# Performance work log

Hardware: AMD Instinct MI355X
Metric: run time of the kernel (lower is better)

## Reference

```python
import jax, jax.numpy as jnp
import numpy as np

B, S, D, H = 2, 2048, 512, 8
DK = D // H  # 64


def setup_inputs() -> dict:
    key = jax.random.key(0)
    ks = jax.random.split(key, 16)
    def t(k):
        return jax.random.normal(k, (B, S, D), dtype=jnp.float32)
    inp = {
        'query_real': t(ks[0]), 'key_real': t(ks[1]), 'value_real': t(ks[2]),
        'query_phase': t(ks[3]), 'key_phase': t(ks[4]), 'value_phase': t(ks[5]),
        'mask': jax.random.randint(ks[6], (B, 1, S), 0, 2, dtype=jnp.int32),
    }
    # Four distinct linear layers (clones deepcopies); real and phase paths share them.
    for i, nm in enumerate(['q', 'k', 'v', 'o']):
        inp['W' + nm] = jax.random.normal(ks[7 + 2 * i], (D, D), dtype=jnp.float32) * 0.02
        inp['b' + nm] = jax.random.normal(ks[8 + 2 * i], (D,), dtype=jnp.float32) * 0.02
    return inp


def _lin(x, W, b):
    # nn.Linear: x @ W.T + b
    return jnp.einsum('bsd,ed->bse', x, W) + b


def _heads(x):
    # [B,S,D] -> [B,H,S,DK]
    return jnp.swapaxes(x.reshape(B, S, H, DK), 1, 2)


def reference(query_real, key_real, value_real, query_phase, key_phase, value_phase,
              mask, Wq, bq, Wk, bk, Wv, bv, Wo, bo):
    qr = _heads(_lin(query_real, Wq, bq)); qp = _heads(_lin(query_phase, Wq, bq))
    kr = _heads(_lin(key_real, Wk, bk));   kp = _heads(_lin(key_phase, Wk, bk))
    vr = _heads(_lin(value_real, Wv, bv)); vp = _heads(_lin(value_phase, Wv, bv))

    # complex QK^T: 4 matmuls -> real/imag parts, magnitude score
    sr = jnp.einsum('bhqd,bhkd->bhqk', qr, kr) - jnp.einsum('bhqd,bhkd->bhqk', qp, kp)
    sp = jnp.einsum('bhqd,bhkd->bhqk', qr, kp) + jnp.einsum('bhqd,bhkd->bhqk', qp, kr)
    scores = jnp.sqrt(sr * sr + sp * sp) / jnp.sqrt(jnp.float32(DK))
    # mask [B,1,S] -> unsqueeze head dim -> [B,1,1,S]
    scores = jnp.where(mask[:, None] == 0, jnp.float32(-1e9), scores)
    p = jax.nn.softmax(scores, axis=-1)

    xr = jnp.einsum('bhqk,bhkd->bhqd', p, vr)
    xp = jnp.einsum('bhqk,bhkd->bhqd', p, vp)
    xr = jnp.swapaxes(xr, 1, 2).reshape(B, S, D)
    xp = jnp.swapaxes(xp, 1, 2).reshape(B, S, D)
    return _lin(xr, Wo, bo), _lin(xp, Wo, bo)
```

## Files before the change

### kernel.cpp

```cpp
#include <hip/hip_runtime.h>

typedef __bf16 bf16;
typedef __bf16 bf16x8 __attribute__((ext_vector_type(8)));
typedef float  f32x4  __attribute__((ext_vector_type(4)));

static constexpr int CB = 2;
static constexpr int CS = 2048;
static constexpr int CD = 512;
static constexpr int CH = 8;
static constexpr int CDK = 64;
static constexpr int NROWS = CB * CH * CS;
static constexpr size_t NT = (size_t)CB * CS * CD;
static constexpr size_t WN = (size_t)CD * CD;

__device__ __forceinline__ f32x4 mfma16(bf16x8 a, bf16x8 b, f32x4 c) {
    return __builtin_amdgcn_mfma_f32_16x16x32_bf16(a, b, c, 0, 0, 0);
}

__device__ __forceinline__ bf16x8 cvt8(const float* __restrict__ p) {
    float4 x0 = *reinterpret_cast<const float4*>(p);
    float4 x1 = *reinterpret_cast<const float4*>(p + 4);
    bf16x8 r;
    r[0] = (bf16)x0.x; r[1] = (bf16)x0.y; r[2] = (bf16)x0.z; r[3] = (bf16)x0.w;
    r[4] = (bf16)x1.x; r[5] = (bf16)x1.y; r[6] = (bf16)x1.z; r[7] = (bf16)x1.w;
    return r;
}

__device__ __forceinline__ void gload16(const void* g, void* l) {
    __builtin_amdgcn_global_load_lds(
        (const __attribute__((address_space(1))) void*)g,
        (__attribute__((address_space(3))) void*)l, 16, 0, 0);
}

struct CvtP {
    const float* src[10];
    bf16* dst[10];
    int n8[10];
};
__global__ __launch_bounds__(256) void cvt_kernel(CvtP C) {
    const int t = blockIdx.y;
    const int i = blockIdx.x * 256 + threadIdx.x;
    if (i < C.n8[t])
        *reinterpret_cast<bf16x8*>(C.dst[t] + (size_t)i * 8) =
            cvt8(C.src[t] + (size_t)i * 8);
}

struct PB {
    const bf16* A[6];
    const bf16* W[6];
    const float* bias[6];
    bf16* dst[6];
    int mode[6];
};
__global__ __launch_bounds__(256) void projb_kernel(PB P) {
    __shared__ uint4 tile[2][2][512];

    const int z = blockIdx.z;
    const bf16* __restrict__ A = P.A[z];
    const bf16* __restrict__ W = P.W[z];
    const float* __restrict__ bias = P.bias[z];
    bf16* __restrict__ dst = P.dst[z];
    const int mode = P.mode[z];

    const int m0 = blockIdx.x * 64, n0 = blockIdx.y * 64;
    const int tid = threadIdx.x;
    const int lane = tid & 63, w = tid >> 6;
    const int wm = w >> 1, wn = w & 1;
    const int l16 = lane & 15, lhi = lane >> 4;

    const int tensor = w >> 1, half = w & 1;
    const int rlo = lane >> 3, slotL = lane & 7;
    const bf16* gbase = tensor ? W : A;
    const int t0 = tensor ? n0 : m0;
    const char* gp = (const char*)gbase
                   + (size_t)(t0 + half*32 + rlo) * (CD * 2)
                   + (size_t)((slotL ^ rlo) * 16);

    auto stage = [&](int buf, int kk) {
        const char* p = gp + (size_t)kk * 128;
        uint4* ld = &tile[buf][tensor][half * 256];
        #pragma unroll
        for (int i = 0; i < 4; ++i)
            gload16(p + (size_t)i * 8 * (CD * 2), ld + i * 64);
    };

    f32x4 acc[2][2] = {};

    stage(0, 0);
    asm volatile("s_waitcnt vmcnt(0)" ::: "memory");
    __syncthreads();

    for (int kk = 0; kk < 8; ++kk) {
        if (kk + 1 < 8) stage((kk + 1) & 1, kk + 1);

        const uint4* aT = &tile[kk & 1][0][0];
        const uint4* bT = &tile[kk & 1][1][0];
        #pragma unroll
        for (int ks = 0; ks < 2; ++ks) {
            const int c = ks*4 + lhi;
            const int ra0 = wm*32 + l16, ra1 = ra0 + 16;
            const int rb0 = wn*32 + l16, rb1 = rb0 + 16;
            bf16x8 af0 = __builtin_bit_cast(bf16x8, aT[ra0*8 + (c ^ (ra0 & 7))]);
            bf16x8 af1 = __builtin_bit_cast(bf16x8, aT[ra1*8 + (c ^ (ra1 & 7))]);
            bf16x8 bg0 = __builtin_bit_cast(bf16x8, bT[rb0*8 + (c ^ (rb0 & 7))]);
            bf16x8 bg1 = __builtin_bit_cast(bf16x8, bT[rb1*8 + (c ^ (rb1 & 7))]);
            acc[0][0] = mfma16(af0, bg0, acc[0][0]);
            acc[0][1] = mfma16(af0, bg1, acc[0][1]);
            acc[1][0] = mfma16(af1, bg0, acc[1][0]);
            acc[1][1] = mfma16(af1, bg1, acc[1][1]);
        }
        if (kk + 1 < 8) __syncthreads();
    }

    #pragma unroll
    for (int ms = 0; ms < 2; ++ms)
    #pragma unroll
    for (int ns = 0; ns < 2; ++ns) {
        const int col = n0 + wn*32 + ns*16 + l16;
        const float bv = bias[col];
        const int hh = col >> 6, dk = col & 63;
        #pragma unroll
        for (int i = 0; i < 4; ++i) {
            const int m = m0 + wm*32 + ms*16 + lhi*4 + i;
            const float v = acc[ms][ns][i] + bv;
            const int b = m >> 11, s = m & 2047;
            if (mode == 0)
                dst[(((size_t)(b*CH + hh)) * CS + s) * CDK + dk] = (bf16)v;
            else
                dst[(((size_t)(b*CH + hh)) * CDK + dk) * CS + s] = (bf16)v;
        }
    }
}

__global__ __launch_bounds__(256) void oprojb_kernel(
    const bf16* __restrict__ Xr, const bf16* __restrict__ Xp,
    const bf16* __restrict__ Wo, const float* __restrict__ bo,
    float* __restrict__ out)
{
    __shared__ uint4 tile[2][2][512];

    const bf16* __restrict__ A = blockIdx.z ? Xp : Xr;
    float* __restrict__ dst = out + (size_t)blockIdx.z * NT;

    const int m0 = blockIdx.x * 64, n0 = blockIdx.y * 64;
    const int tid = threadIdx.x;
    const int lane = tid & 63, w = tid >> 6;
    const int wm = w >> 1, wn = w & 1;
    const int l16 = lane & 15, lhi = lane >> 4;

    const int tensor = w >> 1, half = w & 1;
    const int rlo = lane >> 3, slotL = lane & 7;
    const bf16* gbase = tensor ? Wo : A;
    const int t0 = tensor ? n0 : m0;
    const char* gp = (const char*)gbase
                   + (size_t)(t0 + half*32 + rlo) * (CD * 2)
                   + (size_t)((slotL ^ rlo) * 16);

    auto stage = [&](int buf, int kk) {
        const char* p = gp + (size_t)kk * 128;
        uint4* ld = &tile[buf][tensor][half * 256];
        #pragma unroll
        for (int i = 0; i < 4; ++i)
            gload16(p + (size_t)i * 8 * (CD * 2), ld + i * 64);
    };

    f32x4 acc[2][2] = {};

    stage(0, 0);
    asm volatile("s_waitcnt vmcnt(0)" ::: "memory");
    __syncthreads();

    for (int kk = 0; kk < 8; ++kk) {
        if (kk + 1 < 8) stage((kk + 1) & 1, kk + 1);

        const uint4* aT = &tile[kk & 1][0][0];
        const uint4* bT = &tile[kk & 1][1][0];
        #pragma unroll
        for (int ks = 0; ks < 2; ++ks) {
            const int c = ks*4 + lhi;
            const int ra0 = wm*32 + l16, ra1 = ra0 + 16;
            const int rb0 = wn*32 + l16, rb1 = rb0 + 16;
            bf16x8 af0 = __builtin_bit_cast(bf16x8, aT[ra0*8 + (c ^ (ra0 & 7))]);
            bf16x8 af1 = __builtin_bit_cast(bf16x8, aT[ra1*8 + (c ^ (ra1 & 7))]);
            bf16x8 bg0 = __builtin_bit_cast(bf16x8, bT[rb0*8 + (c ^ (rb0 & 7))]);
            bf16x8 bg1 = __builtin_bit_cast(bf16x8, bT[rb1*8 + (c ^ (rb1 & 7))]);
            acc[0][0] = mfma16(af0, bg0, acc[0][0]);
            acc[0][1] = mfma16(af0, bg1, acc[0][1]);
            acc[1][0] = mfma16(af1, bg0, acc[1][0]);
            acc[1][1] = mfma16(af1, bg1, acc[1][1]);
        }
        if (kk + 1 < 8) __syncthreads();
    }

    #pragma unroll
    for (int ms = 0; ms < 2; ++ms)
    #pragma unroll
    for (int ns = 0; ns < 2; ++ns) {
        const int col = n0 + wn*32 + ns*16 + l16;
        const float bv = bo[col];
        #pragma unroll
        for (int i = 0; i < 4; ++i) {
            const int m = m0 + wm*32 + ms*16 + lhi*4 + i;
            dst[(size_t)m * 512 + col] = acc[ms][ns][i] + bv;
        }
    }
}

__global__ __launch_bounds__(256) void attn_kernel(
    const bf16* __restrict__ Qr, const bf16* __restrict__ Qp,
    const bf16* __restrict__ Kr, const bf16* __restrict__ Kp,
    const bf16* __restrict__ Vtr, const bf16* __restrict__ Vtp,
    const int* __restrict__ mask, int lognsp,
    float* __restrict__ POR, float* __restrict__ POP, float* __restrict__ PLs)
{
    __shared__ uint4 stg[2][4][512];

    const int F = blockIdx.x;
    const int qt = (F >> 3) & 15;
    const int g  = (F & 7) | ((F >> 7) << 3);
    const int bh = g >> lognsp, z = g & ((1 << lognsp) - 1);
    const int Lkv = CS >> lognsp, kvbase = z * Lkv;
    const int nt = Lkv >> 6;
    const int b = bh >> 3;
    const size_t base = (size_t)bh * CS * CDK;

    const int tid = threadIdx.x, lane = tid & 63, w = tid >> 6;
    const int l16 = lane & 15, lhi = lane >> 4;
    const int q0 = qt * 128 + w * 32;

    const int srowL = lane >> 3, slotL = lane & 7;
    const int chunkL = slotL ^ srowL;
    const char* gsrc;
    size_t laneoff, iStride, tStride;
    if (w == 0)      gsrc = (const char*)Kr;
    else if (w == 1) gsrc = (const char*)Kp;
    else if (w == 2) gsrc = (const char*)Vtr;
    else             gsrc = (const char*)Vtp;
    if (w < 2) {
        laneoff = base*2 + (size_t)(kvbase + srowL) * 128 + chunkL*16;
        iStride = 1024;  tStride = 8192;
    } else {
        laneoff = base*2 + (size_t)srowL * (CS*2) + (size_t)kvbase*2 + chunkL*16;
        iStride = 8 * CS * 2;  tStride = 128;
    }
    const char* gp = gsrc + laneoff;

    auto stage = [&](int bi, int t) {
        const char* p = gp + (size_t)t * tStride;
        uint4* ldst = &stg[bi][w][0];
        #pragma unroll
        for (int i = 0; i < 8; ++i)
            gload16(p + i*iStride, ldst + i*64);
    };

    stage(0, 0);

    bf16x8 qrf[2][2], qpf[2][2], qnf[2][2];
    #pragma unroll
    for (int ms = 0; ms < 2; ++ms)
        #pragma unroll
        for (int ks = 0; ks < 2; ++ks) {
            const size_t qoff = base + (size_t)(q0 + ms*16 + l16) * CDK + ks*32 + lhi*8;
            qrf[ms][ks] = *reinterpret_cast<const bf16x8*>(&Qr[qoff]);
            qpf[ms][ks] = *reinterpret_cast<const bf16x8*>(&Qp[qoff]);
            uint4 t = __builtin_bit_cast(uint4, qpf[ms][ks]);
            t.x ^= 0x80008000u; t.y ^= 0x80008000u; t.z ^= 0x80008000u; t.w ^= 0x80008000u;
            qnf[ms][ks] = __builtin_bit_cast(bf16x8, t);
        }

    unsigned long long keepA[8] = {};
    for (int t = 0; t < nt; ++t) {
        const unsigned long long m64 =
            __ballot(mask[b*CS + kvbase + t*64 + lane] != 0);
        const unsigned long long s = m64 >> (lhi * 4);
        const unsigned int k16 = (unsigned int)(s & 0xFull)
                               | ((unsigned int)((s >> 16) & 0xFull) << 4)
                               | ((unsigned int)((s >> 32) & 0xFull) << 8)
                               | ((unsigned int)((s >> 48) & 0xFull) << 12);
        keepA[t >> 2] |= (unsigned long long)k16 << ((t & 3) * 16);
    }

    f32x4 oR[2][4] = {}, oP[2][4] = {};
    float lpart[2] = {0.f, 0.f};

    asm volatile("s_waitcnt vmcnt(0)" ::: "memory");
    __syncthreads();

    for (int t = 0; t < nt; ++t) {
        if (t + 1 < nt) stage((t + 1) & 1, t + 1);

        const int bi = t & 1;
        const unsigned int k16 = (unsigned int)(keepA[t >> 2] >> ((t & 3) * 16)) & 0xFFFFu;
        const uint4* kTr = &stg[bi][0][0];
        const uint4* kTp = &stg[bi][1][0];
        const uint4* vTr = &stg[bi][2][0];
        const uint4* vTp = &stg[bi][3][0];

        #pragma unroll
        for (int ms = 0; ms < 2; ++ms) {
            float pp[4][4];
            #pragma unroll
            for (int kb = 0; kb < 4; ++kb) {
                const int krow = kb*16 + l16;
                f32x4 aR = {}, aP = {};
                __builtin_amdgcn_s_setprio(1);
                #pragma unroll
                for (int ks = 0; ks < 2; ++ks) {
                    const int ci = krow*8 + ((ks*4 + lhi) ^ (krow & 7));
                    const bf16x8 kr8 = __builtin_bit_cast(bf16x8, kTr[ci]);
                    const bf16x8 kp8 = __builtin_bit_cast(bf16x8, kTp[ci]);
                    aR = mfma16(kr8, qrf[ms][ks], aR);
                    aR = mfma16(kp8, qnf[ms][ks], aR);
                    aP = mfma16(kr8, qpf[ms][ks], aP);
                    aP = mfma16(kp8, qrf[ms][ks], aP);
                }
                __builtin_amdgcn_s_setprio(0);
                #pragma unroll
                for (int i = 0; i < 4; ++i) {
                    const float sr = aR[i], sp = aP[i];
                    const float mag = __builtin_amdgcn_sqrtf(fmaf(sr, sr, sp*sp));
                    float p = __builtin_amdgcn_exp2f(fmaf(mag, 0.18033688f, -5.77078016f));
                    p = ((k16 >> (kb*4 + i)) & 1u) ? p : 0.0f;
                    pp[kb][i] = p;
                    lpart[ms] += p;
                }
            }
            #pragma unroll
            for (int c = 0; c < 2; ++c) {
                unsigned int r0, r1, r2, r3;
                asm("v_cvt_pk_bf16_f32 %0, %1, %2" : "=v"(r0) : "v"(pp[2*c][0]),   "v"(pp[2*c][1]));
                asm("v_cvt_pk_bf16_f32 %0, %1, %2" : "=v"(r1) : "v"(pp[2*c][2]),   "v"(pp[2*c][3]));
                asm("v_cvt_pk_bf16_f32 %0, %1, %2" : "=v"(r2) : "v"(pp[2*c+1][0]), "v"(pp[2*c+1][1]));
                asm("v_cvt_pk_bf16_f32 %0, %1, %2" : "=v"(r3) : "v"(pp[2*c+1][2]), "v"(pp[2*c+1][3]));
                asm volatile("v_permlane32_swap_b32 %0, %1" : "+v"(r0), "+v"(r2));
                asm volatile("v_permlane32_swap_b32 %0, %1" : "+v"(r1), "+v"(r3));
                asm volatile("v_permlane16_swap_b32 %0, %1" : "+v"(r0), "+v"(r2));
                asm volatile("v_permlane16_swap_b32 %0, %1" : "+v"(r1), "+v"(r3));
                uint4 fw; fw.x = r0; fw.y = r1; fw.z = r2; fw.w = r3;
                const bf16x8 pa = __builtin_bit_cast(bf16x8, fw);
                __builtin_amdgcn_s_setprio(1);
                #pragma unroll
                for (int dt = 0; dt < 4; ++dt) {
                    const int vrow = dt*16 + l16;
                    const int ci = vrow*8 + ((c*4 + lhi) ^ (vrow & 7));
                    oR[ms][dt] = mfma16(__builtin_bit_cast(bf16x8, vTr[ci]), pa, oR[ms][dt]);
                    oP[ms][dt] = mfma16(__builtin_bit_cast(bf16x8, vTp[ci]), pa, oP[ms][dt]);
                }
                __builtin_amdgcn_s_setprio(0);
            }
        }

        if (t + 1 < nt) __syncthreads();
    }

    #pragma unroll
    for (int ms = 0; ms < 2; ++ms) {
        float v = lpart[ms];
        v += __shfl_xor(v, 16);
        v += __shfl_xor(v, 32);
        lpart[ms] = v;
    }
    const int r0q = bh * CS + q0;
    if (lane < 16) {
        PLs[(size_t)z * NROWS + r0q + lane]      = lpart[0];
        PLs[(size_t)z * NROWS + r0q + 16 + lane] = lpart[1];
    }
    const size_t zo = (size_t)z * NROWS * 64;
    #pragma unroll
    for (int ms = 0; ms < 2; ++ms)
        #pragma unroll
        for (int dt = 0; dt < 4; ++dt) {
            const size_t off = zo + (size_t)(r0q + ms*16 + l16) * 64 + dt*16 + lhi*4;
            *reinterpret_cast<f32x4*>(&POR[off]) = oR[ms][dt];
            *reinterpret_cast<f32x4*>(&POP[off]) = oP[ms][dt];
        }
}

__global__ __launch_bounds__(256) void merge_kernel(
    const float* __restrict__ POR, const float* __restrict__ POP,
    const float* __restrict__ PLs, int nsp,
    bf16* __restrict__ Xr, bf16* __restrict__ Xp)
{
    const int idx = blockIdx.x * 256 + threadIdx.x;
    const int r = idx >> 4, c0 = (idx & 15) * 4;
    float l = 0.f;
    f32x4 orv = {}, opv = {};
    for (int zz = 0; zz < nsp; ++zz) {
        l += PLs[(size_t)zz * NROWS + r];
        const size_t o = (size_t)zz * NROWS * 64 + (size_t)r * 64 + c0;
        orv += *reinterpret_cast<const f32x4*>(&POR[o]);
        opv += *reinterpret_cast<const f32x4*>(&POP[o]);
    }
    const float inv = 1.f / l;
    const int bh = r >> 11, q = r & 2047;
    const int b = bh >> 3, h = bh & 7;
    const size_t off = ((size_t)(b*CS + q)) * CD + h*CDK + c0;
    bf16 vr[4], vp[4];
    #pragma unroll
    for (int j = 0; j < 4; ++j) { vr[j] = (bf16)(orv[j]*inv); vp[j] = (bf16)(opv[j]*inv); }
    *reinterpret_cast<uint2*>(&Xr[off]) = *reinterpret_cast<const uint2*>(vr);
    *reinterpret_cast<uint2*>(&Xp[off]) = *reinterpret_cast<const uint2*>(vp);
}

extern "C" void kernel_launch(void* const* d_in, const int* in_sizes, int n_in,
                              void* d_out, int out_size, void* d_ws, size_t ws_size,
                              hipStream_t stream) {
    const float* q_r = (const float*)d_in[0];
    const float* k_r = (const float*)d_in[1];
    const float* v_r = (const float*)d_in[2];
    const float* q_p = (const float*)d_in[3];
    const float* k_p = (const float*)d_in[4];
    const float* v_p = (const float*)d_in[5];
    const int*  mask = (const int*)d_in[6];
    const float* Wq = (const float*)d_in[7];  const float* bq = (const float*)d_in[8];
    const float* Wk = (const float*)d_in[9];  const float* bk = (const float*)d_in[10];
    const float* Wv = (const float*)d_in[11]; const float* bv = (const float*)d_in[12];
    const float* Wo = (const float*)d_in[13]; const float* bo = (const float*)d_in[14];
    float* out = (float*)d_out;

    bf16* ws = (bf16*)d_ws;
    bf16* Abf = ws;
    bf16* Wbf = ws + 6 * NT;
    bf16* Qr  = Wbf + 4 * WN;
    bf16 *Qp = Qr + NT, *Kr = Qp + NT, *Kp = Kr + NT;
    bf16 *Vtr = Kp + NT, *Vtp = Vtr + NT;
    bf16 *Xr = Vtp + NT, *Xp = Xr + NT;
    float* POR = (float*)(Xp + NT);

    const size_t fixedB = (14 * NT + 4 * WN) * sizeof(bf16);
    const size_t per_split = (size_t)NROWS * 64 * 4 * 2 + (size_t)NROWS * 4;
    int nsp, lognsp;
    if (ws_size >= fixedB + 2 * per_split) { nsp = 2; lognsp = 1; }
    else                                   { nsp = 1; lognsp = 0; }
    float* POP = POR + (size_t)nsp * NROWS * 64;
    float* PLs = POP + (size_t)nsp * NROWS * 64;

    dim3 blk(256);

    CvtP C;
    C.src[0]=q_r; C.src[1]=q_p; C.src[2]=k_r; C.src[3]=k_p; C.src[4]=v_r; C.src[5]=v_p;
    C.src[6]=Wq;  C.src[7]=Wk;  C.src[8]=Wv;  C.src[9]=Wo;
    for (int i = 0; i < 6; ++i) { C.dst[i] = Abf + (size_t)i * NT; C.n8[i] = (int)(NT / 8); }
    for (int i = 0; i < 4; ++i) { C.dst[6+i] = Wbf + (size_t)i * WN; C.n8[6+i] = (int)(WN / 8); }
    cvt_kernel<<<dim3((unsigned)(NT / 8 / 256), 10), blk, 0, stream>>>(C);

    PB P;
    for (int i = 0; i < 6; ++i) P.A[i] = Abf + (size_t)i * NT;
    P.W[0]=Wbf;      P.W[1]=Wbf;      P.W[2]=Wbf+WN;   P.W[3]=Wbf+WN;
    P.W[4]=Wbf+2*WN; P.W[5]=Wbf+2*WN;
    P.bias[0]=bq; P.bias[1]=bq; P.bias[2]=bk; P.bias[3]=bk; P.bias[4]=bv; P.bias[5]=bv;
    P.dst[0]=Qr; P.dst[1]=Qp; P.dst[2]=Kr; P.dst[3]=Kp; P.dst[4]=Vtr; P.dst[5]=Vtp;
    P.mode[0]=0; P.mode[1]=0; P.mode[2]=0; P.mode[3]=0; P.mode[4]=1; P.mode[5]=1;
    projb_kernel<<<dim3(64, 8, 6), blk, 0, stream>>>(P);

    attn_kernel<<<dim3(256 * nsp), blk, 0, stream>>>(Qr, Qp, Kr, Kp, Vtr, Vtp,
                                                     mask, lognsp, POR, POP, PLs);

    merge_kernel<<<dim3(NROWS * 16 / 256), blk, 0, stream>>>(POR, POP, PLs, nsp, Xr, Xp);

    oprojb_kernel<<<dim3(64, 8, 2), blk, 0, stream>>>(Xr, Xp, Wbf + 3 * WN, bo, out);
}
```

Before: 128.6 us.

## Split attention block into 8 waves of 16 query rows each

The attention kernel now runs 512 threads (8 waves) per block instead of 256, and each wave handles 16 query rows rather than 32. K/V tile staging is split so two waves load each tensor half. The aim is more waves in flight to hide the latency of the exp/sqrt and LDS reads, and fewer registers per wave. In exchange, each K/V fragment read from LDS is reused across fewer query rows, so LDS read traffic per MFMA doubles.

```diff
diff --git a/kernel.cpp b/kernel.cpp
--- a/kernel.cpp
+++ b/kernel.cpp
@@ -206,7 +206,7 @@
     }
 }
 
-__global__ __launch_bounds__(256) void attn_kernel(
+__global__ __launch_bounds__(512, 4) void attn_kernel(
     const bf16* __restrict__ Qr, const bf16* __restrict__ Qp,
     const bf16* __restrict__ Kr, const bf16* __restrict__ Kp,
     const bf16* __restrict__ Vtr, const bf16* __restrict__ Vtp,
@@ -226,47 +226,43 @@
 
     const int tid = threadIdx.x, lane = tid & 63, w = tid >> 6;
     const int l16 = lane & 15, lhi = lane >> 4;
-    const int q0 = qt * 128 + w * 32;
-
-    const int srowL = lane >> 3, slotL = lane & 7;
-    const int chunkL = slotL ^ srowL;
-    const char* gsrc;
+    const int q0 = qt * 128 + w * 16;
+
+    const int tensor = w >> 1, half = w & 1;
+    const int rlo = lane >> 3, slotL = lane & 7;
+    const int chunkL = slotL ^ rlo;
+    const char* gsrc = (tensor == 0) ? (const char*)Kr : (tensor == 1) ? (const char*)Kp
+                     : (tensor == 2) ? (const char*)Vtr : (const char*)Vtp;
     size_t laneoff, iStride, tStride;
-    if (w == 0)      gsrc = (const char*)Kr;
-    else if (w == 1) gsrc = (const char*)Kp;
-    else if (w == 2) gsrc = (const char*)Vtr;
-    else             gsrc = (const char*)Vtp;
-    if (w < 2) {
-        laneoff = base*2 + (size_t)(kvbase + srowL) * 128 + chunkL*16;
-        iStride = 1024;  tStride = 8192;
+    if (tensor < 2) {
+        laneoff = base*2 + (size_t)(kvbase + half*32 + rlo) * 128 + chunkL*16;
+        iStride = 8 * 128;  tStride = 8192;
     } else {
-        laneoff = base*2 + (size_t)srowL * (CS*2) + (size_t)kvbase*2 + chunkL*16;
+        laneoff = base*2 + (size_t)(half*32 + rlo) * (CS*2) + (size_t)kvbase*2 + chunkL*16;
         iStride = 8 * CS * 2;  tStride = 128;
     }
     const char* gp = gsrc + laneoff;
 
     auto stage = [&](int bi, int t) {
         const char* p = gp + (size_t)t * tStride;
-        uint4* ldst = &stg[bi][w][0];
-        #pragma unroll
-        for (int i = 0; i < 8; ++i)
+        uint4* ldst = &stg[bi][tensor][half * 256];
+        #pragma unroll
+        for (int i = 0; i < 4; ++i)
             gload16(p + i*iStride, ldst + i*64);
     };
 
     stage(0, 0);
 
-    bf16x8 qrf[2][2], qpf[2][2], qnf[2][2];
-    #pragma unroll
-    for (int ms = 0; ms < 2; ++ms)
-        #pragma unroll
-        for (int ks = 0; ks < 2; ++ks) {
-            const size_t qoff = base + (size_t)(q0 + ms*16 + l16) * CDK + ks*32 + lhi*8;
-            qrf[ms][ks] = *reinterpret_cast<const bf16x8*>(&Qr[qoff]);
-            qpf[ms][ks] = *reinterpret_cast<const bf16x8*>(&Qp[qoff]);
-            uint4 t = __builtin_bit_cast(uint4, qpf[ms][ks]);
-            t.x ^= 0x80008000u; t.y ^= 0x80008000u; t.z ^= 0x80008000u; t.w ^= 0x80008000u;
-            qnf[ms][ks] = __builtin_bit_cast(bf16x8, t);
-        }
+    bf16x8 qrf[2], qpf[2], qnf[2];
+    #pragma unroll
+    for (int ks = 0; ks < 2; ++ks) {
+        const size_t qoff = base + (size_t)(q0 + l16) * CDK + ks*32 + lhi*8;
+        qrf[ks] = *reinterpret_cast<const bf16x8*>(&Qr[qoff]);
+        qpf[ks] = *reinterpret_cast<const bf16x8*>(&Qp[qoff]);
+        uint4 t = __builtin_bit_cast(uint4, qpf[ks]);
+        t.x ^= 0x80008000u; t.y ^= 0x80008000u; t.z ^= 0x80008000u; t.w ^= 0x80008000u;
+        qnf[ks] = __builtin_bit_cast(bf16x8, t);
+    }
 
     unsigned long long keepA[8] = {};
     for (int t = 0; t < nt; ++t) {
@@ -280,8 +276,8 @@
         keepA[t >> 2] |= (unsigned long long)k16 << ((t & 3) * 16);
     }
 
-    f32x4 oR[2][4] = {}, oP[2][4] = {};
-    float lpart[2] = {0.f, 0.f};
+    f32x4 oR[4] = {}, oP[4] = {};
+    float lpart = 0.f;
 
     asm volatile("s_waitcnt vmcnt(0)" ::: "memory");
     __syncthreads();
@@ -296,84 +292,78 @@
         const uint4* vTr = &stg[bi][2][0];
         const uint4* vTp = &stg[bi][3][0];
 
-        #pragma unroll
-        for (int ms = 0; ms < 2; ++ms) {
-            float pp[4][4];
+        float pp[4][4];
+        #pragma unroll
+        for (int kb = 0; kb < 4; ++kb) {
+            const int krow = kb*16 + l16;
+            f32x4 aR = {}, aP = {};
+            __builtin_amdgcn_s_setprio(1);
             #pragma unroll
-            for (int kb = 0; kb < 4; ++kb) {
-                const int krow = kb*16 + l16;
-                f32x4 aR = {}, aP = {};
-                __builtin_amdgcn_s_setprio(1);
-                #pragma unroll
-                for (int ks = 0; ks < 2; ++ks) {
-                    const int ci = krow*8 + ((ks*4 + lhi) ^ (krow & 7));
-                    const bf16x8 kr8 = __builtin_bit_cast(bf16x8, kTr[ci]);
-                    const bf16x8 kp8 = __builtin_bit_cast(bf16x8, kTp[ci]);
-                    aR = mfma16(kr8, qrf[ms][ks], aR);
-                    aR = mfma16(kp8, qnf[ms][ks], aR);
-                    aP = mfma16(kr8, qpf[ms][ks], aP);
-                    aP = mfma16(kp8, qrf[ms][ks], aP);
-                }
-                __builtin_amdgcn_s_setprio(0);
-                #pragma unroll
-                for (int i = 0; i < 4; ++i) {
-                    const float sr = aR[i], sp = aP[i];
-                    const float mag = __builtin_amdgcn_sqrtf(fmaf(sr, sr, sp*sp));
-                    float p = __builtin_amdgcn_exp2f(fmaf(mag, 0.18033688f, -5.77078016f));
-                    p = ((k16 >> (kb*4 + i)) & 1u) ? p : 0.0f;
-                    pp[kb][i] = p;
-                    lpart[ms] += p;
-                }
+            for (int ks = 0; ks < 2; ++ks) {
+                const int ci = krow*8 + ((ks*4 + lhi) ^ (krow & 7));
+                const bf16x8 kr8 = __builtin_bit_cast(bf16x8, kTr[ci]);
+                const bf16x8 kp8 = __builtin_bit_cast(bf16x8, kTp[ci]);
+                aR = mfma16(kr8, qrf[ks], aR);
+                aR = mfma16(kp8, qnf[ks], aR);
+                aP = mfma16(kr8, qpf[ks], aP);
+                aP = mfma16(kp8, qrf[ks], aP);
             }
+            __builtin_amdgcn_s_setprio(0);
             #pragma unroll
-            for (int c = 0; c < 2; ++c) {
-                unsigned int r0, r1, r2, r3;
-                asm("v_cvt_pk_bf16_f32 %0, %1, %2" : "=v"(r0) : "v"(pp[2*c][0]),   "v"(pp[2*c][1]));
-                asm("v_cvt_pk_bf16_f32 %0, %1, %2" : "=v"(r1) : "v"(pp[2*c][2]),   "v"(pp[2*c][3]));
-                asm("v_cvt_pk_bf16_f32 %0, %1, %2" : "=v"(r2) : "v"(pp[2*c+1][0]), "v"(pp[2*c+1][1]));
-                asm("v_cvt_pk_bf16_f32 %0, %1, %2" : "=v"(r3) : "v"(pp[2*c+1][2]), "v"(pp[2*c+1][3]));
-                asm volatile("v_permlane32_swap_b32 %0, %1" : "+v"(r0), "+v"(r2));
-                asm volatile("v_permlane32_swap_b32 %0, %1" : "+v"(r1), "+v"(r3));
-                asm volatile("v_permlane16_swap_b32 %0, %1" : "+v"(r0), "+v"(r2));
-                asm volatile("v_permlane16_swap_b32 %0, %1" : "+v"(r1), "+v"(r3));
-                uint4 fw; fw.x = r0; fw.y = r1; fw.z = r2; fw.w = r3;
-                const bf16x8 pa = __builtin_bit_cast(bf16x8, fw);
-                __builtin_amdgcn_s_setprio(1);
-                #pragma unroll
-                for (int dt = 0; dt < 4; ++dt) {
-                    const int vrow = dt*16 + l16;
-                    const int ci = vrow*8 + ((c*4 + lhi) ^ (vrow & 7));
-                    oR[ms][dt] = mfma16(__builtin_bit_cast(bf16x8, vTr[ci]), pa, oR[ms][dt]);
-                    oP[ms][dt] = mfma16(__builtin_bit_cast(bf16x8, vTp[ci]), pa, oP[ms][dt]);
-                }
-                __builtin_amdgcn_s_setprio(0);
+            for (int i = 0; i < 4; ++i) {
+                const float sr = aR[i], sp = aP[i];
+                const float mag = __builtin_amdgcn_sqrtf(fmaf(sr, sr, sp*sp));
+                float p = __builtin_amdgcn_exp2f(fmaf(mag, 0.18033688f, -5.77078016f));
+                p = ((k16 >> (kb*4 + i)) & 1u) ? p : 0.0f;
+                pp[kb][i] = p;
+                lpart += p;
             }
         }
 
+        #pragma unroll
+        for (int c = 0; c < 2; ++c) {
+            unsigned int r0, r1, r2, r3;
+            asm("v_cvt_pk_bf16_f32 %0, %1, %2" : "=v"(r0) : "v"(pp[2*c][0]),   "v"(pp[2*c][1]));
+            asm("v_cvt_pk_bf16_f32 %0, %1, %2" : "=v"(r1) : "v"(pp[2*c][2]),   "v"(pp[2*c][3]));
+            asm("v_cvt_pk_bf16_f32 %0, %1, %2" : "=v"(r2) : "v"(pp[2*c+1][0]), "v"(pp[2*c+1][1]));
+            asm("v_cvt_pk_bf16_f32 %0, %1, %2" : "=v"(r3) : "v"(pp[2*c+1][2]), "v"(pp[2*c+1][3]));
+            asm volatile("v_permlane32_swap_b32 %0, %1" : "+v"(r0), "+v"(r2));
+            asm volatile("v_permlane32_swap_b32 %0, %1" : "+v"(r1), "+v"(r3));
+            asm volatile("v_permlane16_swap_b32 %0, %1" : "+v"(r0), "+v"(r2));
+            asm volatile("v_permlane16_swap_b32 %0, %1" : "+v"(r1), "+v"(r3));
+            uint4 fw; fw.x = r0; fw.y = r1; fw.z = r2; fw.w = r3;
+            const bf16x8 pa = __builtin_bit_cast(bf16x8, fw);
+            __builtin_amdgcn_s_setprio(1);
+            #pragma unroll
+            for (int dt = 0; dt < 4; ++dt) {
+                const int vrow = dt*16 + l16;
+                const int ci = vrow*8 + ((c*4 + lhi) ^ (vrow & 7));
+                oR[dt] = mfma16(__builtin_bit_cast(bf16x8, vTr[ci]), pa, oR[dt]);
+                oP[dt] = mfma16(__builtin_bit_cast(bf16x8, vTp[ci]), pa, oP[dt]);
+            }
+            __builtin_amdgcn_s_setprio(0);
+        }
+
         if (t + 1 < nt) __syncthreads();
     }
 
-    #pragma unroll
-    for (int ms = 0; ms < 2; ++ms) {
-        float v = lpart[ms];
+    {
+        float v = lpart;
         v += __shfl_xor(v, 16);
         v += __shfl_xor(v, 32);
-        lpart[ms] = v;
+        lpart = v;
     }
     const int r0q = bh * CS + q0;
-    if (lane < 16) {
-        PLs[(size_t)z * NROWS + r0q + lane]      = lpart[0];
-        PLs[(size_t)z * NROWS + r0q + 16 + lane] = lpart[1];
-    }
+    if (lane < 16)
+        PLs[(size_t)z * NROWS + r0q + lane] = lpart;
+
     const size_t zo = (size_t)z * NROWS * 64;
     #pragma unroll
-    for (int ms = 0; ms < 2; ++ms)
-        #pragma unroll
-        for (int dt = 0; dt < 4; ++dt) {
-            const size_t off = zo + (size_t)(r0q + ms*16 + l16) * 64 + dt*16 + lhi*4;
-            *reinterpret_cast<f32x4*>(&POR[off]) = oR[ms][dt];
-            *reinterpret_cast<f32x4*>(&POP[off]) = oP[ms][dt];
-        }
+    for (int dt = 0; dt < 4; ++dt) {
+        const size_t off = zo + (size_t)(r0q + l16) * 64 + dt*16 + lhi*4;
+        *reinterpret_cast<f32x4*>(&POR[off]) = oR[dt];
+        *reinterpret_cast<f32x4*>(&POP[off]) = oP[dt];
+    }
 }
 
 __global__ __launch_bounds__(256) void merge_kernel(
@@ -453,8 +443,8 @@
     P.mode[0]=0; P.mode[1]=0; P.mode[2]=0; P.mode[3]=0; P.mode[4]=1; P.mode[5]=1;
     projb_kernel<<<dim3(64, 8, 6), blk, 0, stream>>>(P);
 
-    attn_kernel<<<dim3(256 * nsp), blk, 0, stream>>>(Qr, Qp, Kr, Kp, Vtr, Vtp,
-                                                     mask, lognsp, POR, POP, PLs);
+    attn_kernel<<<dim3(256 * nsp), dim3(512), 0, stream>>>(Qr, Qp, Kr, Kp, Vtr, Vtp,
+                                                           mask, lognsp, POR, POP, PLs);
 
     merge_kernel<<<dim3(NROWS * 16 / 256), blk, 0, stream>>>(POR, POP, PLs, nsp, Xr, Xp);
 
```

Result: faster. 122.7 us (-4.6%).

## Split K/V LDS staging, single-buffer V, and interchange ms/kb loops

Applied to the files above, without the earlier changes.

Restructures the attention kernel's LDS staging. K stays double-buffered, V is now single-buffered and loaded during the QK/softmax phase, which cuts the LDS footprint and allows an occupancy hint of 3 blocks per SM. The loops are interchanged so each K/V fragment read from LDS feeds both query sub-tiles, and the sign flip for the imaginary term moves from Q to K. Barriers are split into two per iteration with explicit vmcnt waits, and the last iteration redundantly reloads tile 0 of K. This adds synchronisation and raises register pressure from holding more live accumulators.

```diff
diff --git a/kernel.cpp b/kernel.cpp
--- a/kernel.cpp
+++ b/kernel.cpp
@@ -206,14 +206,15 @@
     }
 }
 
-__global__ __launch_bounds__(256) void attn_kernel(
+__global__ __launch_bounds__(256, 3) void attn_kernel(
     const bf16* __restrict__ Qr, const bf16* __restrict__ Qp,
     const bf16* __restrict__ Kr, const bf16* __restrict__ Kp,
     const bf16* __restrict__ Vtr, const bf16* __restrict__ Vtp,
     const int* __restrict__ mask, int lognsp,
     float* __restrict__ POR, float* __restrict__ POP, float* __restrict__ PLs)
 {
-    __shared__ uint4 stg[2][4][512];
+    __shared__ uint4 kbuf[2][2][512];
+    __shared__ uint4 vbuf[2][512];
 
     const int F = blockIdx.x;
     const int qt = (F >> 3) & 15;
@@ -228,34 +229,33 @@
     const int l16 = lane & 15, lhi = lane >> 4;
     const int q0 = qt * 128 + w * 32;
 
-    const int srowL = lane >> 3, slotL = lane & 7;
-    const int chunkL = slotL ^ srowL;
-    const char* gsrc;
-    size_t laneoff, iStride, tStride;
-    if (w == 0)      gsrc = (const char*)Kr;
-    else if (w == 1) gsrc = (const char*)Kp;
-    else if (w == 2) gsrc = (const char*)Vtr;
-    else             gsrc = (const char*)Vtp;
-    if (w < 2) {
-        laneoff = base*2 + (size_t)(kvbase + srowL) * 128 + chunkL*16;
-        iStride = 1024;  tStride = 8192;
-    } else {
-        laneoff = base*2 + (size_t)srowL * (CS*2) + (size_t)kvbase*2 + chunkL*16;
-        iStride = 8 * CS * 2;  tStride = 128;
-    }
-    const char* gp = gsrc + laneoff;
-
-    auto stage = [&](int bi, int t) {
-        const char* p = gp + (size_t)t * tStride;
-        uint4* ldst = &stg[bi][w][0];
-        #pragma unroll
-        for (int i = 0; i < 8; ++i)
-            gload16(p + i*iStride, ldst + i*64);
+    const int ktensor = w & 1, half = w >> 1;
+    const int rlo = lane >> 3, slotL = lane & 7;
+    const int chunkL = slotL ^ rlo;
+    const char* kgsrc = ktensor ? (const char*)Kp : (const char*)Kr;
+    const char* vgsrc = ktensor ? (const char*)Vtp : (const char*)Vtr;
+    const char* kgp = kgsrc + base*2 + (size_t)(kvbase + half*32 + rlo) * 128 + chunkL*16;
+    const char* vgp = vgsrc + base*2 + (size_t)(half*32 + rlo) * (CS*2)
+                    + (size_t)kvbase*2 + chunkL*16;
+
+    auto stageK = [&](int bi, int t) {
+        const char* p = kgp + (size_t)t * 8192;
+        uint4* ld = &kbuf[bi][ktensor][half * 256];
+        #pragma unroll
+        for (int i = 0; i < 4; ++i)
+            gload16(p + (size_t)i * (8*128), ld + i*64);
     };
-
-    stage(0, 0);
-
-    bf16x8 qrf[2][2], qpf[2][2], qnf[2][2];
+    auto stageV = [&](int t) {
+        const char* p = vgp + (size_t)t * 128;
+        uint4* ld = &vbuf[ktensor][half * 256];
+        #pragma unroll
+        for (int i = 0; i < 4; ++i)
+            gload16(p + (size_t)i * (8*CS*2), ld + i*64);
+    };
+
+    stageK(0, 0);
+
+    bf16x8 qrf[2][2], qpf[2][2];
     #pragma unroll
     for (int ms = 0; ms < 2; ++ms)
         #pragma unroll
@@ -263,9 +263,6 @@
             const size_t qoff = base + (size_t)(q0 + ms*16 + l16) * CDK + ks*32 + lhi*8;
             qrf[ms][ks] = *reinterpret_cast<const bf16x8*>(&Qr[qoff]);
             qpf[ms][ks] = *reinterpret_cast<const bf16x8*>(&Qp[qoff]);
-            uint4 t = __builtin_bit_cast(uint4, qpf[ms][ks]);
-            t.x ^= 0x80008000u; t.y ^= 0x80008000u; t.z ^= 0x80008000u; t.w ^= 0x80008000u;
-            qnf[ms][ks] = __builtin_bit_cast(bf16x8, t);
         }
 
     unsigned long long keepA[8] = {};
@@ -287,70 +284,95 @@
     __syncthreads();
 
     for (int t = 0; t < nt; ++t) {
-        if (t + 1 < nt) stage((t + 1) & 1, t + 1);
-
-        const int bi = t & 1;
+        stageV(t);
+        stageK((t + 1) & 1, (t + 1 < nt) ? t + 1 : 0);
+
         const unsigned int k16 = (unsigned int)(keepA[t >> 2] >> ((t & 3) * 16)) & 0xFFFFu;
-        const uint4* kTr = &stg[bi][0][0];
-        const uint4* kTp = &stg[bi][1][0];
-        const uint4* vTr = &stg[bi][2][0];
-        const uint4* vTp = &stg[bi][3][0];
-
-        #pragma unroll
-        for (int ms = 0; ms < 2; ++ms) {
-            float pp[4][4];
+        const uint4* kTr = &kbuf[t & 1][0][0];
+        const uint4* kTp = &kbuf[t & 1][1][0];
+
+        float pp[2][4][4];
+        #pragma unroll
+        for (int kb = 0; kb < 4; ++kb) {
+            const int krow = kb*16 + l16;
+            f32x4 aR[2] = {}, aP[2] = {};
             #pragma unroll
-            for (int kb = 0; kb < 4; ++kb) {
-                const int krow = kb*16 + l16;
-                f32x4 aR = {}, aP = {};
+            for (int ks = 0; ks < 2; ++ks) {
+                const int ci = krow*8 + ((ks*4 + lhi) ^ (krow & 7));
+                const bf16x8 kr8 = __builtin_bit_cast(bf16x8, kTr[ci]);
+                const bf16x8 kp8 = __builtin_bit_cast(bf16x8, kTp[ci]);
+                uint4 tn = __builtin_bit_cast(uint4, kp8);
+                tn.x ^= 0x80008000u; tn.y ^= 0x80008000u;
+                tn.z ^= 0x80008000u; tn.w ^= 0x80008000u;
+                const bf16x8 kn8 = __builtin_bit_cast(bf16x8, tn);
                 __builtin_amdgcn_s_setprio(1);
                 #pragma unroll
-                for (int ks = 0; ks < 2; ++ks) {
-                    const int ci = krow*8 + ((ks*4 + lhi) ^ (krow & 7));
-                    const bf16x8 kr8 = __builtin_bit_cast(bf16x8, kTr[ci]);
-                    const bf16x8 kp8 = __builtin_bit_cast(bf16x8, kTp[ci]);
-                    aR = mfma16(kr8, qrf[ms][ks], aR);
-                    aR = mfma16(kp8, qnf[ms][ks], aR);
-                    aP = mfma16(kr8, qpf[ms][ks], aP);
-                    aP = mfma16(kp8, qrf[ms][ks], aP);
+                for (int ms = 0; ms < 2; ++ms) {
+                    aR[ms] = mfma16(kr8, qrf[ms][ks], aR[ms]);
+                    aR[ms] = mfma16(kn8, qpf[ms][ks], aR[ms]);
+                    aP[ms] = mfma16(kr8, qpf[ms][ks], aP[ms]);
+                    aP[ms] = mfma16(kp8, qrf[ms][ks], aP[ms]);
                 }
                 __builtin_amdgcn_s_setprio(0);
+            }
+            #pragma unroll
+            for (int ms = 0; ms < 2; ++ms)
                 #pragma unroll
                 for (int i = 0; i < 4; ++i) {
-                    const float sr = aR[i], sp = aP[i];
+                    const float sr = aR[ms][i], sp = aP[ms][i];
                     const float mag = __builtin_amdgcn_sqrtf(fmaf(sr, sr, sp*sp));
                     float p = __builtin_amdgcn_exp2f(fmaf(mag, 0.18033688f, -5.77078016f));
                     p = ((k16 >> (kb*4 + i)) & 1u) ? p : 0.0f;
-                    pp[kb][i] = p;
+                    pp[ms][kb][i] = p;
                     lpart[ms] += p;
                 }
-            }
+        }
+
+        bf16x8 pa[2][2];
+        #pragma unroll
+        for (int c = 0; c < 2; ++c)
             #pragma unroll
-            for (int c = 0; c < 2; ++c) {
+            for (int ms = 0; ms < 2; ++ms) {
                 unsigned int r0, r1, r2, r3;
-                asm("v_cvt_pk_bf16_f32 %0, %1, %2" : "=v"(r0) : "v"(pp[2*c][0]),   "v"(pp[2*c][1]));
-                asm("v_cvt_pk_bf16_f32 %0, %1, %2" : "=v"(r1) : "v"(pp[2*c][2]),   "v"(pp[2*c][3]));
-                asm("v_cvt_pk_bf16_f32 %0, %1, %2" : "=v"(r2) : "v"(pp[2*c+1][0]), "v"(pp[2*c+1][1]));
-                asm("v_cvt_pk_bf16_f32 %0, %1, %2" : "=v"(r3) : "v"(pp[2*c+1][2]), "v"(pp[2*c+1][3]));
+                asm("v_cvt_pk_bf16_f32 %0, %1, %2" : "=v"(r0) : "v"(pp[ms][2*c][0]),   "v"(pp[ms][2*c][1]));
+                asm("v_cvt_pk_bf16_f32 %0, %1, %2" : "=v"(r1) : "v"(pp[ms][2*c][2]),   "v"(pp[ms][2*c][3]));
+                asm("v_cvt_pk_bf16_f32 %0, %1, %2" : "=v"(r2) : "v"(pp[ms][2*c+1][0]), "v"(pp[ms][2*c+1][1]));
+                asm("v_cvt_pk_bf16_f32 %0, %1, %2" : "=v"(r3) : "v"(pp[ms][2*c+1][2]), "v"(pp[ms][2*c+1][3]));
                 asm volatile("v_permlane32_swap_b32 %0, %1" : "+v"(r0), "+v"(r2));
                 asm volatile("v_permlane32_swap_b32 %0, %1" : "+v"(r1), "+v"(r3));
                 asm volatile("v_permlane16_swap_b32 %0, %1" : "+v"(r0), "+v"(r2));
                 asm volatile("v_permlane16_swap_b32 %0, %1" : "+v"(r1), "+v"(r3));
                 uint4 fw; fw.x = r0; fw.y = r1; fw.z = r2; fw.w = r3;
-                const bf16x8 pa = __builtin_bit_cast(bf16x8, fw);
-                __builtin_amdgcn_s_setprio(1);
+                pa[c][ms] = __builtin_bit_cast(bf16x8, fw);
+            }
+
+        asm volatile("s_waitcnt vmcnt(4)" ::: "memory");
+        __builtin_amdgcn_sched_barrier(0);
+        __builtin_amdgcn_s_barrier();
+        __builtin_amdgcn_sched_barrier(0);
+
+        #pragma unroll
+        for (int c = 0; c < 2; ++c) {
+            __builtin_amdgcn_s_setprio(1);
+            #pragma unroll
+            for (int dt = 0; dt < 4; ++dt) {
+                const int vrow = dt*16 + l16;
+                const int ci = vrow*8 + ((c*4 + lhi) ^ (vrow & 7));
+                const bf16x8 v8r = __builtin_bit_cast(bf16x8, vbuf[0][ci]);
+                const bf16x8 v8p = __builtin_bit_cast(bf16x8, vbuf[1][ci]);
                 #pragma unroll
-                for (int dt = 0; dt < 4; ++dt) {
-                    const int vrow = dt*16 + l16;
-                    const int ci = vrow*8 + ((c*4 + lhi) ^ (vrow & 7));
-                    oR[ms][dt] = mfma16(__builtin_bit_cast(bf16x8, vTr[ci]), pa, oR[ms][dt]);
-                    oP[ms][dt] = mfma16(__builtin_bit_cast(bf16x8, vTp[ci]), pa, oP[ms][dt]);
+                for (int ms = 0; ms < 2; ++ms) {
+                    oR[ms][dt] = mfma16(v8r, pa[c][ms], oR[ms][dt]);
+                    oP[ms][dt] = mfma16(v8p, pa[c][ms], oP[ms][dt]);
                 }
-                __builtin_amdgcn_s_setprio(0);
             }
-        }
-
-        if (t + 1 < nt) __syncthreads();
+            __builtin_amdgcn_s_setprio(0);
+        }
+
+        asm volatile("s_waitcnt vmcnt(0)" ::: "memory");
+        __builtin_amdgcn_sched_barrier(0);
+        __builtin_amdgcn_s_barrier();
+        __builtin_amdgcn_sched_barrier(0);
     }
 
     #pragma unroll
```

Result: slower. 134.6 us (+4.7%).
